# Optimization experiments

Measured on AMD Instinct MI355X. Metric: run time of the kernel, lower is better.

The kernel has to match this reference:

```python
import jax, jax.numpy as jnp
import numpy as np

B = 8
INPUT_SHAPE = (32, 32)
OUTPUT_SHAPE = (64, 64)
NDIMS = len(INPUT_SHAPE)


def setup_inputs() -> dict:
    key = jax.random.key(0)
    k1, k2 = jax.random.split(key)
    y = jax.random.normal(k1, (B, *INPUT_SHAPE), dtype=jnp.float32)
    xnew = jax.random.uniform(k2, (B, *OUTPUT_SHAPE, NDIMS), dtype=jnp.float32)
    return {"y": y, "xnew": xnew}


def reference(y, xnew):
    # y: (B, D0, D1); xnew: (B, O0, O1, 2) in [0, 1]
    fft_shape = y.shape[1:]
    b = y.shape[0]
    n = int(np.prod(OUTPUT_SHAPE))  # n_sample_points
    dims = jnp.asarray(fft_shape, dtype=jnp.float32)

    # scale sample points to [0, dim-1] as in the torch code
    sp = xnew.reshape(b, n, NDIMS) * jnp.clip(dims - 1.0, 0.0)  # (B, N, 2)

    # frequency-index grid m[i,j,d] = idx_d / D_d, shape (D0, D1, 2)
    grids = jnp.meshgrid(*[jnp.arange(d, dtype=jnp.float32) for d in fft_shape], indexing="ij")
    m = jnp.stack(grids, axis=-1) / dims

    # phase[b,i,j,n] = 2*pi * sum_d m[i,j,d] * sp[b,n,d]
    phase = (2.0 * jnp.pi) * jnp.einsum("ijd,bnd->bijn", m, sp)

    F = jnp.fft.fftn(y.astype(jnp.complex64), axes=(1, 2))  # (B, D0, D1)
    Fr, Fi = jnp.real(F), jnp.imag(F)

    # Real part of mean_{i,j} F[b,i,j] * exp(i*phase[b,i,j,n]):
    #   mean(Fr*cos(phase) - Fi*sin(phase)) over the (D0, D1) frequency bins.
    num = jnp.einsum("bij,bijn->bn", Fr, jnp.cos(phase)) - jnp.einsum("bij,bijn->bn", Fi, jnp.sin(phase))
    out = num / jnp.float32(np.prod(fft_shape))  # (B, N)
    return out.reshape(b, *OUTPUT_SHAPE)
```

## Files before the change

### kernel.cpp

```cpp
#include <hip/hip_runtime.h>
#include <math.h>

#define PI_F   3.14159265358979f
#define PIO32  0.0981747704246810f

constexpr float CT[32] = {
  1.0f,          0.995184727f,  0.980785280f,  0.956940336f,
  0.923879533f,  0.881921264f,  0.831469612f,  0.773010453f,
  0.707106781f,  0.634393284f,  0.555570233f,  0.471396737f,
  0.382683432f,  0.290284677f,  0.195090322f,  0.0980171403f,
  0.0f,         -0.0980171403f, -0.195090322f, -0.290284677f,
 -0.382683432f, -0.471396737f, -0.555570233f, -0.634393284f,
 -0.707106781f, -0.773010453f, -0.831469612f, -0.881921264f,
 -0.923879533f, -0.956940336f, -0.980785280f, -0.995184727f };
constexpr float ST[32] = {
  0.0f,          0.0980171403f, 0.195090322f,  0.290284677f,
  0.382683432f,  0.471396737f,  0.555570233f,  0.634393284f,
  0.707106781f,  0.773010453f,  0.831469612f,  0.881921264f,
  0.923879533f,  0.956940336f,  0.980785280f,  0.995184727f,
  1.0f,          0.995184727f,  0.980785280f,  0.956940336f,
  0.923879533f,  0.881921264f,  0.831469612f,  0.773010453f,
  0.707106781f,  0.634393284f,  0.555570233f,  0.471396737f,
  0.382683432f,  0.290284677f,  0.195090322f,  0.0980171403f };

struct Dim {
  float K;
  float Cr, Ci;
  float sth, cth;
  float spole;
  int   pstar;
};

__device__ inline Dim dimcalc(float sp) {
  Dim d;
  const float ps = rintf(sp);
  d.pstar = (int)ps;
  float dstar = sp - ps;
  if (dstar == 0.0f) dstar = 1e-10f;
  const float th = sp * PIO32;
  d.sth = __sinf(th);
  d.cth = __cosf(th);
  const float pd = PI_F * dstar;
  const float sd = __sinf(pd);
  const float cd = __cosf(pd);
  const float par = (d.pstar & 1) ? -1.0f : 1.0f;
  d.K = par * sd;
  d.Cr = par * fmaf(cd, d.cth, sd * d.sth);
  d.Ci = par * fmaf(sd, d.cth, -cd * d.sth);
  const float x = dstar * PIO32;
  const float x2 = x * x;
  d.spole = x * fmaf(x2, fmaf(x2, 0.00833333333f, -0.166666667f), 1.0f);
  return d;
}

__global__ __launch_bounds__(256) void fourier_interp_kernel(
    const float* __restrict__ y, const float* __restrict__ xnew,
    float* __restrict__ out) {
  const int tid = threadIdx.x;
  const int gid = blockIdx.x * 256 + tid;
  const int h  = gid & 3;
  const int pt = gid >> 2;
  const int b  = pt >> 12;

  const float2 x2v = ((const float2*)xnew)[pt];
  const Dim d0 = dimcalc(x2v.x * 31.0f);
  const Dim d1 = dimcalc(x2v.y * 31.0f);

  float Gr[32], Gi[32];
#pragma unroll
  for (int q = 0; q < 32; ++q) {
    float s = fmaf(d1.sth, CT[q], -d1.cth * ST[q]);
    if (q == d1.pstar) s = d1.spole;
    const float t = d1.K * __builtin_amdgcn_rcpf(s);
    Gr[q] = t * CT[q];
    Gi[q] = t * ST[q];
  }

  const float e4r = (h == 0) ? 1.f : (h == 1) ? 0.707106781f
                  : (h == 2) ? 0.f : -0.707106781f;
  const float e4i = (h == 0) ? 0.f : (h == 1) ? 0.707106781f
                  : (h == 2) ? 1.f : 0.707106781f;
  const int p0 = h * 8;
  float Hr[8], Hi[8];
#pragma unroll
  for (int pp = 0; pp < 8; ++pp) {
    const float Tr = fmaf(e4r, CT[pp], -e4i * ST[pp]);
    const float Ti = fmaf(e4r, ST[pp],  e4i * CT[pp]);
    float s = fmaf(d0.sth, Tr, -d0.cth * Ti);
    if (p0 + pp == d0.pstar) s = d0.spole;
    const float t = d0.K * __builtin_amdgcn_rcpf(s);
    Hr[pp] = t * Tr;
    Hi[pp] = t * Ti;
  }

  const float4* yr = (const float4*)(y + b * 1024 + p0 * 32);
  float Zr = 0.f, Zi = 0.f;
#pragma unroll 2
  for (int pp = 0; pp < 8; ++pp) {
    float SrA = 0.f, SrB = 0.f, SiA = 0.f, SiB = 0.f;
#pragma unroll
    for (int q4 = 0; q4 < 8; ++q4) {
      const float4 v = yr[pp * 8 + q4];
      SrA = fmaf(v.x, Gr[4 * q4 + 0], SrA); SiA = fmaf(v.x, Gi[4 * q4 + 0], SiA);
      SrB = fmaf(v.y, Gr[4 * q4 + 1], SrB); SiB = fmaf(v.y, Gi[4 * q4 + 1], SiB);
      SrA = fmaf(v.z, Gr[4 * q4 + 2], SrA); SiA = fmaf(v.z, Gi[4 * q4 + 2], SiA);
      SrB = fmaf(v.w, Gr[4 * q4 + 3], SrB); SiB = fmaf(v.w, Gi[4 * q4 + 3], SiB);
    }
    const float Sr = SrA + SrB;
    const float Si = SiA + SiB;
    Zr = fmaf(Hr[pp], Sr, Zr); Zr = fmaf(-Hi[pp], Si, Zr);
    Zi = fmaf(Hr[pp], Si, Zi); Zi = fmaf(Hi[pp], Sr, Zi);
  }

  Zr += __shfl_xor(Zr, 1); Zr += __shfl_xor(Zr, 2);
  Zi += __shfl_xor(Zi, 1); Zi += __shfl_xor(Zi, 2);
  const float Cr = fmaf(d0.Cr, d1.Cr, -d0.Ci * d1.Ci);
  const float Ci = fmaf(d0.Cr, d1.Ci,  d0.Ci * d1.Cr);
  const float res = fmaf(Cr, Zr, -Ci * Zi) * (1.0f / 1024.0f);

  const int l = tid & 63;
  const float packed = __shfl(res, (l & 15) * 4);
  if (l < 16) {
    const int wbase = (blockIdx.x * 256 + (tid & ~63)) >> 2;
    out[wbase + l] = packed;
  }
}

extern "C" void kernel_launch(void* const* d_in, const int* in_sizes, int n_in,
                              void* d_out, int out_size, void* d_ws, size_t ws_size,
                              hipStream_t stream) {
  const float* y    = (const float*)d_in[0];
  const float* xnew = (const float*)d_in[1];
  float* out = (float*)d_out;
  (void)d_ws; (void)ws_size;

  hipLaunchKernelGGL(fourier_interp_kernel, dim3(512), dim3(256), 0, stream,
                     y, xnew, out);
}
```

Baseline: 70.30 us.

## Interchange loops to compute column weights on the fly and cut register use

Swaps the loop order so the 32 column weights (Gr/Gi) are generated four at a time inside the column loop, with eight row accumulators kept live instead of 64 precomputed weights. The row weights (Hr/Hi) are computed and applied right after the column loop. This is meant to lower VGPR pressure and raise occupancy or avoid spills. In exchange the sums use a different order and there are 16 live accumulators.

```diff
diff --git a/kernel.cpp b/kernel.cpp
--- a/kernel.cpp
+++ b/kernel.cpp
@@ -31,7 +31,7 @@
   int   pstar;
 };
 
-__device__ inline Dim dimcalc(float sp) {
+__device__ __forceinline__ Dim dimcalc(float sp) {
   Dim d;
   const float ps = rintf(sp);
   d.pstar = (int)ps;
@@ -66,51 +66,79 @@
   const Dim d0 = dimcalc(x2v.x * 31.0f);
   const Dim d1 = dimcalc(x2v.y * 31.0f);
 
-  float Gr[32], Gi[32];
+  const int p0 = h * 8;
+  const float* ybase = y + b * 1024 + p0 * 32;
+
+  float S0r = 0.f, S0i = 0.f, S1r = 0.f, S1i = 0.f;
+  float S2r = 0.f, S2i = 0.f, S3r = 0.f, S3i = 0.f;
+  float S4r = 0.f, S4i = 0.f, S5r = 0.f, S5i = 0.f;
+  float S6r = 0.f, S6i = 0.f, S7r = 0.f, S7i = 0.f;
+
+#define GCOL(c, gr, gi)                                            \
+  float gr, gi;                                                    \
+  {                                                                \
+    float s_ = fmaf(d1.sth, CT[c], -d1.cth * ST[c]);               \
+    if ((c) == d1.pstar) s_ = d1.spole;                            \
+    const float t_ = d1.K * __builtin_amdgcn_rcpf(s_);             \
+    gr = t_ * CT[c];                                               \
+    gi = t_ * ST[c];                                               \
+  }
+
+#define ROWACC(r, Sr_, Si_)                                        \
+  {                                                                \
+    const float4 v = *(const float4*)(ybase + (r) * 32 + 4 * q4);  \
+    Sr_ = fmaf(v.x, g0r, Sr_); Si_ = fmaf(v.x, g0i, Si_);          \
+    Sr_ = fmaf(v.y, g1r, Sr_); Si_ = fmaf(v.y, g1i, Si_);          \
+    Sr_ = fmaf(v.z, g2r, Sr_); Si_ = fmaf(v.z, g2i, Si_);          \
+    Sr_ = fmaf(v.w, g3r, Sr_); Si_ = fmaf(v.w, g3i, Si_);          \
+  }
+
 #pragma unroll
-  for (int q = 0; q < 32; ++q) {
-    float s = fmaf(d1.sth, CT[q], -d1.cth * ST[q]);
-    if (q == d1.pstar) s = d1.spole;
-    const float t = d1.K * __builtin_amdgcn_rcpf(s);
-    Gr[q] = t * CT[q];
-    Gi[q] = t * ST[q];
+  for (int q4 = 0; q4 < 8; ++q4) {
+    GCOL(4 * q4 + 0, g0r, g0i)
+    GCOL(4 * q4 + 1, g1r, g1i)
+    GCOL(4 * q4 + 2, g2r, g2i)
+    GCOL(4 * q4 + 3, g3r, g3i)
+    ROWACC(0, S0r, S0i)
+    ROWACC(1, S1r, S1i)
+    ROWACC(2, S2r, S2i)
+    ROWACC(3, S3r, S3i)
+    ROWACC(4, S4r, S4i)
+    ROWACC(5, S5r, S5i)
+    ROWACC(6, S6r, S6i)
+    ROWACC(7, S7r, S7i)
   }
+#undef GCOL
+#undef ROWACC
 
   const float e4r = (h == 0) ? 1.f : (h == 1) ? 0.707106781f
                   : (h == 2) ? 0.f : -0.707106781f;
   const float e4i = (h == 0) ? 0.f : (h == 1) ? 0.707106781f
                   : (h == 2) ? 1.f : 0.707106781f;
-  const int p0 = h * 8;
-  float Hr[8], Hi[8];
-#pragma unroll
-  for (int pp = 0; pp < 8; ++pp) {
-    const float Tr = fmaf(e4r, CT[pp], -e4i * ST[pp]);
-    const float Ti = fmaf(e4r, ST[pp],  e4i * CT[pp]);
-    float s = fmaf(d0.sth, Tr, -d0.cth * Ti);
-    if (p0 + pp == d0.pstar) s = d0.spole;
-    const float t = d0.K * __builtin_amdgcn_rcpf(s);
-    Hr[pp] = t * Tr;
-    Hi[pp] = t * Ti;
+  float Zr = 0.f, Zi = 0.f;
+
+#define HROW(r, Sr_, Si_)                                          \
+  {                                                                \
+    const float Tr = fmaf(e4r, CT[r], -e4i * ST[r]);               \
+    const float Ti = fmaf(e4r, ST[r],  e4i * CT[r]);               \
+    float s_ = fmaf(d0.sth, Tr, -d0.cth * Ti);                     \
+    if (p0 + (r) == d0.pstar) s_ = d0.spole;                       \
+    const float t_ = d0.K * __builtin_amdgcn_rcpf(s_);             \
+    const float Hr_ = t_ * Tr;                                     \
+    const float Hi_ = t_ * Ti;                                     \
+    Zr = fmaf(Hr_, Sr_, Zr); Zr = fmaf(-Hi_, Si_, Zr);             \
+    Zi = fmaf(Hr_, Si_, Zi); Zi = fmaf(Hi_, Sr_, Zi);              \
   }
 
-  const float4* yr = (const float4*)(y + b * 1024 + p0 * 32);
-  float Zr = 0.f, Zi = 0.f;
-#pragma unroll 2
-  for (int pp = 0; pp < 8; ++pp) {
-    float SrA = 0.f, SrB = 0.f, SiA = 0.f, SiB = 0.f;
-#pragma unroll
-    for (int q4 = 0; q4 < 8; ++q4) {
-      const float4 v = yr[pp * 8 + q4];
-      SrA = fmaf(v.x, Gr[4 * q4 + 0], SrA); SiA = fmaf(v.x, Gi[4 * q4 + 0], SiA);
-      SrB = fmaf(v.y, Gr[4 * q4 + 1], SrB); SiB = fmaf(v.y, Gi[4 * q4 + 1], SiB);
-      SrA = fmaf(v.z, Gr[4 * q4 + 2], SrA); SiA = fmaf(v.z, Gi[4 * q4 + 2], SiA);
-      SrB = fmaf(v.w, Gr[4 * q4 + 3], SrB); SiB = fmaf(v.w, Gi[4 * q4 + 3], SiB);
-    }
-    const float Sr = SrA + SrB;
-    const float Si = SiA + SiB;
-    Zr = fmaf(Hr[pp], Sr, Zr); Zr = fmaf(-Hi[pp], Si, Zr);
-    Zi = fmaf(Hr[pp], Si, Zi); Zi = fmaf(Hi[pp], Sr, Zi);
-  }
+  HROW(0, S0r, S0i)
+  HROW(1, S1r, S1i)
+  HROW(2, S2r, S2i)
+  HROW(3, S3r, S3i)
+  HROW(4, S4r, S4i)
+  HROW(5, S5r, S5i)
+  HROW(6, S6r, S6i)
+  HROW(7, S7r, S7i)
+#undef HROW
 
   Zr += __shfl_xor(Zr, 1); Zr += __shfl_xor(Zr, 2);
   Zi += __shfl_xor(Zi, 1); Zi += __shfl_xor(Zi, 2);
```

Result: faster. 68.81 us (-2.1%).

## Split column weights across quad lanes and compute row weights inline

Applied to the files above, without the earlier changes.

The work split among the four lanes handling a point changes. Each lane previously held all 32 column weights and 8 row weights. Now each lane computes only 8 column weights (4 low, 4 high via the quarter-turn identity) and loops over all 32 rows, computing each row weight inline. This is meant to cut register pressure and the duplicated per-lane column-weight setup, which could raise occupancy. The cost is 32 row-weight reciprocals per lane instead of 8, and y loads that are no longer contiguous per lane.

```diff
diff --git a/kernel.cpp b/kernel.cpp
--- a/kernel.cpp
+++ b/kernel.cpp
@@ -31,7 +31,7 @@
   int   pstar;
 };
 
-__device__ inline Dim dimcalc(float sp) {
+__device__ __forceinline__ Dim dimcalc(float sp) {
   Dim d;
   const float ps = rintf(sp);
   d.pstar = (int)ps;
@@ -66,50 +66,73 @@
   const Dim d0 = dimcalc(x2v.x * 31.0f);
   const Dim d1 = dimcalc(x2v.y * 31.0f);
 
-  float Gr[32], Gi[32];
-#pragma unroll
-  for (int q = 0; q < 32; ++q) {
-    float s = fmaf(d1.sth, CT[q], -d1.cth * ST[q]);
-    if (q == d1.pstar) s = d1.spole;
-    const float t = d1.K * __builtin_amdgcn_rcpf(s);
-    Gr[q] = t * CT[q];
-    Gi[q] = t * ST[q];
+  const float e8r = (h == 0) ? 1.f : (h == 1) ? 0.923879533f
+                  : (h == 2) ? 0.707106781f : 0.382683432f;
+  const float e8i = (h == 0) ? 0.f : (h == 1) ? 0.382683432f
+                  : (h == 2) ? 0.707106781f : 0.923879533f;
+
+  const float T0r = e8r;
+  const float T0i = e8i;
+  const float T1r = fmaf(e8r, CT[1], -e8i * ST[1]);
+  const float T1i = fmaf(e8r, ST[1],  e8i * CT[1]);
+  const float T2r = fmaf(e8r, CT[2], -e8i * ST[2]);
+  const float T2i = fmaf(e8r, ST[2],  e8i * CT[2]);
+  const float T3r = fmaf(e8r, CT[3], -e8i * ST[3]);
+  const float T3i = fmaf(e8r, ST[3],  e8i * CT[3]);
+
+#define GLO(j, Tjr, Tji, gr, gi)                                   \
+  float gr, gi;                                                    \
+  {                                                                \
+    float s_ = fmaf(d1.sth, Tjr, -d1.cth * Tji);                   \
+    if (4 * h + (j) == d1.pstar) s_ = d1.spole;                    \
+    const float t_ = d1.K * __builtin_amdgcn_rcpf(s_);             \
+    gr = t_ * Tjr;                                                 \
+    gi = t_ * Tji;                                                 \
+  }
+#define GHI(j, Tjr, Tji, gr, gi)                                   \
+  float gr, gi;                                                    \
+  {                                                                \
+    float s_ = -fmaf(d1.sth, Tji, d1.cth * Tjr);                   \
+    if (16 + 4 * h + (j) == d1.pstar) s_ = d1.spole;               \
+    const float t_ = d1.K * __builtin_amdgcn_rcpf(s_);             \
+    gr = -t_ * Tji;                                                \
+    gi =  t_ * Tjr;                                                \
   }
 
-  const float e4r = (h == 0) ? 1.f : (h == 1) ? 0.707106781f
-                  : (h == 2) ? 0.f : -0.707106781f;
-  const float e4i = (h == 0) ? 0.f : (h == 1) ? 0.707106781f
-                  : (h == 2) ? 1.f : 0.707106781f;
-  const int p0 = h * 8;
-  float Hr[8], Hi[8];
+  GLO(0, T0r, T0i, gl0r, gl0i)
+  GLO(1, T1r, T1i, gl1r, gl1i)
+  GLO(2, T2r, T2i, gl2r, gl2i)
+  GLO(3, T3r, T3i, gl3r, gl3i)
+  GHI(0, T0r, T0i, gh0r, gh0i)
+  GHI(1, T1r, T1i, gh1r, gh1i)
+  GHI(2, T2r, T2i, gh2r, gh2i)
+  GHI(3, T3r, T3i, gh3r, gh3i)
+#undef GLO
+#undef GHI
+
+  const float* ybase = y + b * 1024 + h * 4;
+  float Zr = 0.f, Zi = 0.f;
 #pragma unroll
-  for (int pp = 0; pp < 8; ++pp) {
-    const float Tr = fmaf(e4r, CT[pp], -e4i * ST[pp]);
-    const float Ti = fmaf(e4r, ST[pp],  e4i * CT[pp]);
-    float s = fmaf(d0.sth, Tr, -d0.cth * Ti);
-    if (p0 + pp == d0.pstar) s = d0.spole;
-    const float t = d0.K * __builtin_amdgcn_rcpf(s);
-    Hr[pp] = t * Tr;
-    Hi[pp] = t * Ti;
-  }
-
-  const float4* yr = (const float4*)(y + b * 1024 + p0 * 32);
-  float Zr = 0.f, Zi = 0.f;
-#pragma unroll 2
-  for (int pp = 0; pp < 8; ++pp) {
-    float SrA = 0.f, SrB = 0.f, SiA = 0.f, SiB = 0.f;
-#pragma unroll
-    for (int q4 = 0; q4 < 8; ++q4) {
-      const float4 v = yr[pp * 8 + q4];
-      SrA = fmaf(v.x, Gr[4 * q4 + 0], SrA); SiA = fmaf(v.x, Gi[4 * q4 + 0], SiA);
-      SrB = fmaf(v.y, Gr[4 * q4 + 1], SrB); SiB = fmaf(v.y, Gi[4 * q4 + 1], SiB);
-      SrA = fmaf(v.z, Gr[4 * q4 + 2], SrA); SiA = fmaf(v.z, Gi[4 * q4 + 2], SiA);
-      SrB = fmaf(v.w, Gr[4 * q4 + 3], SrB); SiB = fmaf(v.w, Gi[4 * q4 + 3], SiB);
-    }
+  for (int r = 0; r < 32; ++r) {
+    const float4 v0 = *(const float4*)(ybase + r * 32);
+    const float4 v1 = *(const float4*)(ybase + r * 32 + 16);
+    float SrA = v0.x * gl0r;  SrA = fmaf(v0.z, gl2r, SrA);
+    SrA = fmaf(v1.x, gh0r, SrA); SrA = fmaf(v1.z, gh2r, SrA);
+    float SrB = v0.y * gl1r;  SrB = fmaf(v0.w, gl3r, SrB);
+    SrB = fmaf(v1.y, gh1r, SrB); SrB = fmaf(v1.w, gh3r, SrB);
+    float SiA = v0.x * gl0i;  SiA = fmaf(v0.z, gl2i, SiA);
+    SiA = fmaf(v1.x, gh0i, SiA); SiA = fmaf(v1.z, gh2i, SiA);
+    float SiB = v0.y * gl1i;  SiB = fmaf(v0.w, gl3i, SiB);
+    SiB = fmaf(v1.y, gh1i, SiB); SiB = fmaf(v1.w, gh3i, SiB);
     const float Sr = SrA + SrB;
     const float Si = SiA + SiB;
-    Zr = fmaf(Hr[pp], Sr, Zr); Zr = fmaf(-Hi[pp], Si, Zr);
-    Zi = fmaf(Hr[pp], Si, Zi); Zi = fmaf(Hi[pp], Sr, Zi);
+    float s_ = fmaf(d0.sth, CT[r], -d0.cth * ST[r]);
+    if (r == d0.pstar) s_ = d0.spole;
+    const float t_ = d0.K * __builtin_amdgcn_rcpf(s_);
+    const float Hr = t_ * CT[r];
+    const float Hi = t_ * ST[r];
+    Zr = fmaf(Hr, Sr, Zr); Zr = fmaf(-Hi, Si, Zr);
+    Zi = fmaf(Hr, Si, Zi); Zi = fmaf(Hi, Sr, Zi);
   }
 
   Zr += __shfl_xor(Zr, 1); Zr += __shfl_xor(Zr, 2);
```

Result: faster. 60.27 us (-14.3%).
